# Optimization experiments

Hardware: AMD Instinct MI355X
Metric: run time of the kernel (lower is better)

## Reference

```python
import jax, jax.numpy as jnp
import numpy as np

DIM = 512
NUM_HEADS = 8
HEAD_DIM = DIM // NUM_HEADS
SCALE = HEAD_DIM ** -0.5
HIDDEN = int(DIM * 4.0)
LN_EPS = 1e-5


def layer_norm(x, w, b):
    mu = jnp.mean(x, axis=-1, keepdims=True)
    var = jnp.var(x, axis=-1, keepdims=True)
    return (x - mu) * jax.lax.rsqrt(var + LN_EPS) * w + b


def setup_inputs() -> dict:
    key = jax.random.key(0)
    ks = jax.random.split(key, 8)
    s = 0.02
    return {
        "x": jax.random.normal(ks[0], (8, 4096, DIM), dtype=jnp.float32),
        "ln1_w": jnp.ones((DIM,), jnp.float32),
        "ln1_b": jnp.zeros((DIM,), jnp.float32),
        "qkv_w": jax.random.normal(ks[1], (3 * DIM, DIM), jnp.float32) * s,
        "proj_w": jax.random.normal(ks[2], (DIM, DIM), jnp.float32) * s,
        "proj_b": jnp.zeros((DIM,), jnp.float32),
        "ln2_w": jnp.ones((DIM,), jnp.float32),
        "ln2_b": jnp.zeros((DIM,), jnp.float32),
        "fc1_w": jax.random.normal(ks[3], (HIDDEN, DIM), jnp.float32) * s,
        "fc1_b": jnp.zeros((HIDDEN,), jnp.float32),
        "fc2_w": jax.random.normal(ks[4], (DIM, HIDDEN), jnp.float32) * s,
        "fc2_b": jnp.zeros((DIM,), jnp.float32),
        "eca_w": jax.random.normal(ks[5], (1, 1, 3), jnp.float32) * 0.5,
    }


def channel_attention(x, qkv_w, proj_w, proj_b):
    B, N, C = x.shape
    qkv = (x @ qkv_w.T).reshape(B, N, 3, NUM_HEADS, HEAD_DIM)
    qkv = qkv.transpose(2, 0, 3, 1, 4)  # (3, B, h, N, hd)
    q, k, v = qkv[0], qkv[1] * SCALE, qkv[2]
    # cross-covariance attention: (hd x hd) per head
    attn = jax.nn.softmax(jnp.einsum("bhnd,bhne->bhde", k, v), axis=-1)
    out = jnp.einsum("bhde,bhne->bhnd", attn, q)  # (B, h, N, hd)
    out = out.transpose(0, 2, 1, 3).reshape(B, N, C)
    return out @ proj_w.T + proj_b


def mlp_eca(x, fc1_w, fc1_b, fc2_w, fc2_b, eca_w):
    B, N, C = x.shape
    H = W = int(np.sqrt(N))
    h = jax.nn.gelu(x @ fc1_w.T + fc1_b, approximate=False)
    y = h @ fc2_w.T + fc2_b  # (B, N, C)
    # faithful replication of torch .view(B, C, H, W) on contiguous (B, N, C)
    y4 = y.reshape(B, C, H, W)
    pooled = jnp.mean(y4, axis=(2, 3))  # (B, C)
    conv = jax.lax.conv_general_dilated(
        pooled[:, None, :], eca_w, window_strides=(1,), padding=[(1, 1)],
        dimension_numbers=("NCW", "OIW", "NCW"))[:, 0, :]  # (B, C)
    gate = jax.nn.sigmoid(conv)[:, :, None, None]
    y4 = y4 * gate + y4
    return y4.reshape(B, C, H * W).transpose(0, 2, 1)  # (B, N, C)


def reference(x, ln1_w, ln1_b, qkv_w, proj_w, proj_b, ln2_w, ln2_b,
              fc1_w, fc1_b, fc2_w, fc2_b, eca_w):
    cur = layer_norm(x, ln1_w, ln1_b)
    x = x + channel_attention(cur, qkv_w, proj_w, proj_b)
    x = x + mlp_eca(layer_norm(x, ln2_w, ln2_b), fc1_w, fc1_b, fc2_w, fc2_b, eca_w)
    return x
```

## Files before the change

kernel.cpp:

```cpp
#include <hip/hip_runtime.h>
#include <hip/hip_bf16.h>

typedef __bf16 bf16;
typedef __bf16 bf16x8 __attribute__((ext_vector_type(8)));
typedef float floatx4 __attribute__((ext_vector_type(4)));

#define B_    8
#define N_    4096
#define C_    512
#define BN_   32768
#define HID_  2048
#define SCALE_ 0.125f

__device__ __forceinline__ void load_lds16(const void* g, void* l) {
    __builtin_amdgcn_global_load_lds(
        (const __attribute__((address_space(1))) void*)g,
        (__attribute__((address_space(3))) void*)l, 16, 0, 0);
}

__device__ __forceinline__ float gelu_fast(float v) {
    float c = fmaf(v * v, 0.044715f, 1.0f) * v;
    float e = __builtin_amdgcn_exp2f(-2.3022082f * c);
    return v * __builtin_amdgcn_rcpf(1.0f + e);
}

__global__ void sniff_kernel(const unsigned int* __restrict__ xw, int* __restrict__ flag)
{
    int t = threadIdx.x;
    int votes = 0;
#pragma unroll
    for (int i = 0; i < 4; i++) {
        unsigned w = xw[t * 4 + i];
        if (w == 0u) continue;
        unsigned a = w & 0xFFFFu;
        unsigned e = (a >> 7) & 0xFFu;
        if (a != 0u && e >= 110u && e <= 135u) votes++; else votes--;
    }
#pragma unroll
    for (int off = 32; off; off >>= 1) votes += __shfl_xor(votes, off);
    __shared__ int s[4];
    if ((t & 63) == 0) s[t >> 6] = votes;
    __syncthreads();
    if (t == 0) *flag = (s[0] + s[1] + s[2] + s[3]) > 0 ? 1 : 0;
}

struct ConvArgs {
    const void* src[12];
    unsigned    dstoff[12];
    int         n[12];
};

__global__ __launch_bounds__(256) void convert_params(
    ConvArgs args, char* __restrict__ ws, const int* __restrict__ flag)
{
    int seg = blockIdx.y;
    int n = args.n[seg];
    int base = blockIdx.x * 2048;
    if (base >= n) return;
    bf16* dst = (bf16*)(ws + args.dstoff[seg]);
    const void* src = args.src[seg];
    bool isbf = (*flag != 0);
#pragma unroll
    for (int j = 0; j < 8; j++) {
        int idx = base + threadIdx.x + j * 256;
        if (idx < n) {
            float v = isbf ? (float)((const bf16*)src)[idx]
                           : ((const float*)src)[idx];
            dst[idx] = (bf16)v;
        }
    }
}

__device__ __forceinline__ void ln_core(float f[8], const bf16* w, const bf16* b,
                                        int lane, bf16* outp)
{
    float s = 0.f, sq = 0.f;
#pragma unroll
    for (int j = 0; j < 8; j++) { s += f[j]; sq += f[j]*f[j]; }
#pragma unroll
    for (int off = 32; off; off >>= 1) { s += __shfl_xor(s, off); sq += __shfl_xor(sq, off); }
    float mean = s * (1.f/512.f);
    float var  = sq * (1.f/512.f) - mean*mean;
    float inv  = rsqrtf(var + 1e-5f);
    bf16x8 wv = *(const bf16x8*)(w + lane*8);
    bf16x8 bv = *(const bf16x8*)(b + lane*8);
    bf16x8 o;
#pragma unroll
    for (int j = 0; j < 8; j++) o[j] = (bf16)((f[j]-mean)*inv*(float)wv[j] + (float)bv[j]);
    *(bf16x8*)outp = o;
}

__global__ __launch_bounds__(256) void ln_dyn_kernel(
    const void* __restrict__ xv, const bf16* __restrict__ w,
    const bf16* __restrict__ b, bf16* __restrict__ out, const int* __restrict__ flag)
{
    int wave = threadIdx.x >> 6, lane = threadIdx.x & 63;
    size_t row = (size_t)blockIdx.x * 4 + wave;
    float f[8];
    if (*flag) {
        bf16x8 v = *(const bf16x8*)((const bf16*)xv + row * C_ + lane * 8);
#pragma unroll
        for (int j = 0; j < 8; j++) f[j] = (float)v[j];
    } else {
        const float4* p = (const float4*)((const float*)xv + row * C_ + lane * 8);
        float4 v0 = p[0], v1 = p[1];
        f[0]=v0.x; f[1]=v0.y; f[2]=v0.z; f[3]=v0.w;
        f[4]=v1.x; f[5]=v1.y; f[6]=v1.z; f[7]=v1.w;
    }
    ln_core(f, w, b, lane, out + row * C_ + lane*8);
}

__global__ __launch_bounds__(256) void ln_b16_kernel(
    const bf16* __restrict__ x, const bf16* __restrict__ w,
    const bf16* __restrict__ b, bf16* __restrict__ out)
{
    int wave = threadIdx.x >> 6, lane = threadIdx.x & 63;
    size_t row = (size_t)blockIdx.x * 4 + wave;
    bf16x8 v = *(const bf16x8*)(x + row * C_ + lane * 8);
    float f[8];
#pragma unroll
    for (int j = 0; j < 8; j++) f[j] = (float)v[j];
    ln_core(f, w, b, lane, out + row * C_ + lane*8);
}

__global__ __launch_bounds__(256) void ln_f32_kernel(
    const float* __restrict__ x, const bf16* __restrict__ w,
    const bf16* __restrict__ b, bf16* __restrict__ out)
{
    int wave = threadIdx.x >> 6, lane = threadIdx.x & 63;
    size_t row = (size_t)blockIdx.x * 4 + wave;
    const float4* p = (const float4*)(x + row * C_ + lane * 8);
    float4 v0 = p[0], v1 = p[1];
    float f[8] = { v0.x, v0.y, v0.z, v0.w, v1.x, v1.y, v1.z, v1.w };
    ln_core(f, w, b, lane, out + row * C_ + lane*8);
}

enum { EPI_NONE = 0, EPI_BIAS = 1, EPI_BIAS_RESID = 2, EPI_BIAS_GELU = 3, EPI_QKV = 4 };

#define MM(AF, BF, AH, BH)                                                     \
    __builtin_amdgcn_s_setprio(1);                                             \
    _Pragma("unroll") for (int mi = 0; mi < 4; mi++)                           \
    _Pragma("unroll") for (int ni = 0; ni < 2; ni++)                           \
    _Pragma("unroll") for (int ks = 0; ks < 2; ks++)                           \
        acc[(AH)*4+mi][(BH)*2+ni] = __builtin_amdgcn_mfma_f32_16x16x32_bf16(   \
            AF[mi][ks], BF[ni][ks], acc[(AH)*4+mi][(BH)*2+ni], 0, 0, 0);       \
    __builtin_amdgcn_s_setprio(0);
#define STAGE2(GB, LB)                                                         \
    { load_lds16((GB) + goff0, (LB) + loff0);                                  \
      load_lds16((GB) + goff1, (LB) + loff1); }

#define KTILE(KT, S)                                                           \
{                                                                              \
    bf16x8 af[4][2], bf0[2][2], bf1[2][2];                                     \
                         \
    _Pragma("unroll") for (int mi = 0; mi < 4; mi++)                           \
    _Pragma("unroll") for (int ks = 0; ks < 2; ks++)                           \
        af[mi][ks] = *(const bf16x8*)(pa[mi][ks] + (S) * 16384);               \
    _Pragma("unroll") for (int ni = 0; ni < 2; ni++)                           \
    _Pragma("unroll") for (int ks = 0; ks < 2; ks++)                           \
        bf0[ni][ks] = *(const bf16x8*)(pb[ni][ks] + (S) * 16384);              \
    { const bf16* sp = ((KT) + 1 < NKT)                                        \
          ? A + (size_t)(m0 + 128) * K + (size_t)((KT) + 1) * 64               \
          : (hn ? A + (size_t)(m0n + 128) * K : nullptr);                      \
      if (sp) STAGE2(sp, &Asl[(S) ^ 1][1][0][0]); }                            \
    __builtin_amdgcn_s_barrier();                                              \
    asm volatile("s_waitcnt lgkmcnt(0)");                                      \
    __builtin_amdgcn_sched_barrier(0);                                         \
    MM(af, bf0, 0, 0)                                                          \
                             \
    _Pragma("unroll") for (int ni = 0; ni < 2; ni++)                           \
    _Pragma("unroll") for (int ks = 0; ks < 2; ks++)                           \
        bf1[ni][ks] = *(const bf16x8*)(pb[ni][ks] + (S) * 16384 + 8192);       \
    { const bf16* sp = ((KT) + 1 < NKT)                                        \
          ? W + (size_t)(n0 + 128) * K + (size_t)((KT) + 1) * 64               \
          : (hn ? W + (size_t)(n0n + 128) * K : nullptr);                      \
      if (sp) STAGE2(sp, &Bsl[(S) ^ 1][1][0][0]); }                            \
    __builtin_amdgcn_s_barrier();                                              \
    asm volatile("s_waitcnt lgkmcnt(0)");                                      \
    __builtin_amdgcn_sched_barrier(0);                                         \
    MM(af, bf1, 0, 1)                                                          \
                            \
    _Pragma("unroll") for (int mi = 0; mi < 4; mi++)                           \
    _Pragma("unroll") for (int ks = 0; ks < 2; ks++)                           \
        af[mi][ks] = *(const bf16x8*)(pa[mi][ks] + (S) * 16384 + 8192);        \
    { const bf16* sp = ((KT) + 2 < NKT)                                        \
          ? A + (size_t)m0 * K + (size_t)((KT) + 2) * 64                       \
          : (hn ? A + (size_t)m0n * K + (size_t)((KT) + 2 - NKT) * 64          \
               : nullptr);                                                     \
      if (sp) STAGE2(sp, &Asl[(S)][0][0][0]); }                                \
    __builtin_amdgcn_s_barrier();                                              \
    asm volatile("s_waitcnt lgkmcnt(0)");                                      \
    __builtin_amdgcn_sched_barrier(0);                                         \
    MM(af, bf1, 1, 1)                                                          \
               \
    { const bf16* sp = ((KT) + 2 < NKT)                                        \
          ? W + (size_t)n0 * K + (size_t)((KT) + 2) * 64                       \
          : (hn ? W + (size_t)n0n * K + (size_t)((KT) + 2 - NKT) * 64          \
               : nullptr);                                                     \
      if (sp) STAGE2(sp, &Bsl[(S)][0][0][0]); }                                \
    if ((KT) + 1 < NKT || hn) {                                                \
        if ((KT) + 2 < NKT || hn) asm volatile("s_waitcnt vmcnt(4)");          \
        else                      asm volatile("s_waitcnt vmcnt(0)");          \
    }                                                                          \
    __builtin_amdgcn_s_barrier();                                              \
    MM(af, bf0, 1, 0)                                                          \
}

template<typename OutT, int EPI>
__global__ __launch_bounds__(512, 2) void gemm256(
    const bf16* __restrict__ A, const bf16* __restrict__ W,
    const bf16* __restrict__ bias, const void* __restrict__ resid,
    const int* __restrict__ flag,
    OutT* __restrict__ Cout, bf16* __restrict__ Cout2, int M, int Nn, int K)
{
    __shared__ bf16 Asl[2][2][128][64];
    __shared__ bf16 Bsl[2][2][128][64];
    const int t = threadIdx.x;
    const int wv = t >> 6, lane = t & 63;
    const int quad = lane >> 4, l16 = lane & 15;
    const int wm = wv >> 2, wn = wv & 3;
    const int Nt = Nn >> 8;
    const int total = (M >> 8) * Nt;
    const int G = gridDim.x;
    const int NKT = K >> 6;

    const bf16* pa[4][2];
    const bf16* pb[2][2];
#pragma unroll
    for (int mi = 0; mi < 4; mi++) {
        int row = wm * 64 + mi * 16 + l16;
#pragma unroll
        for (int ks = 0; ks < 2; ks++)
            pa[mi][ks] = &Asl[0][0][0][0] + row * 64 +
                         ((ks * 32 + quad * 8) ^ ((row & 7) << 3));
    }
#pragma unroll
    for (int ni = 0; ni < 2; ni++) {
        int row = wn * 32 + ni * 16 + l16;
#pragma unroll
        for (int ks = 0; ks < 2; ks++)
            pb[ni][ks] = &Bsl[0][0][0][0] + row * 64 +
                         ((ks * 32 + quad * 8) ^ ((row & 7) << 3));
    }

    const int c0 = t, c1 = 512 + t;
    const int r0 = c0 >> 3, r1 = c1 >> 3;
    const size_t goff0 = (size_t)r0 * K + (size_t)(((c0 & 7) ^ (r0 & 7)) * 8);
    const size_t goff1 = (size_t)r1 * K + (size_t)(((c1 & 7) ^ (r1 & 7)) * 8);
    const int loff0 = c0 * 8, loff1 = c1 * 8;

    int id = blockIdx.x;
    if (id >= total) return;
    int m0 = (((id >> 3) / Nt) * 8 + (id & 7)) * 256;
    int n0 = ((id >> 3) % Nt) * 256;

    STAGE2(A + (size_t)m0 * K,         &Asl[0][0][0][0]);
    STAGE2(W + (size_t)n0 * K,         &Bsl[0][0][0][0]);
    STAGE2(A + (size_t)(m0 + 128) * K, &Asl[0][1][0][0]);
    STAGE2(W + (size_t)(n0 + 128) * K, &Bsl[0][1][0][0]);
    STAGE2(A + (size_t)m0 * K + 64,    &Asl[1][0][0][0]);
    STAGE2(W + (size_t)n0 * K + 64,    &Bsl[1][0][0][0]);
    asm volatile("s_waitcnt vmcnt(4)");
    __builtin_amdgcn_s_barrier();

    for (;;) {
        const int idn = id + G;
        const bool hn = idn < total;
        int m0n = 0, n0n = 0;
        if (hn) {
            m0n = (((idn >> 3) / Nt) * 8 + (idn & 7)) * 256;
            n0n = ((idn >> 3) % Nt) * 256;
        }

        floatx4 acc[8][4] = {};

        for (int kt = 0; kt < NKT; kt += 2) {
            KTILE(kt, 0)
            KTILE(kt + 1, 1)
        }

        size_t ldc = (size_t)Nn; int csub = 0; bool to2 = false;
        if (EPI == EPI_QKV) {
            if (n0 >= 512) { to2 = true; ldc = 1024; csub = 512; }
            else           { ldc = 512; }
        }
        bool isbf = false;
        if (EPI == EPI_BIAS_RESID) isbf = (*flag != 0);

#pragma unroll
        for (int mg = 0; mg < 8; mg++) {
            int rowg = m0 + (mg >> 2) * 128 + wm * 64 + (mg & 3) * 16 + quad * 4;
#pragma unroll
            for (int ng = 0; ng < 4; ng++) {
                int col = n0 + (ng >> 1) * 128 + wn * 32 + (ng & 1) * 16 + l16;
                float bv = (EPI == EPI_BIAS || EPI == EPI_BIAS_RESID || EPI == EPI_BIAS_GELU)
                           ? (float)bias[col] : 0.f;
#pragma unroll
                for (int r = 0; r < 4; r++) {
                    size_t idx = (size_t)(rowg + r) * ldc + (col - csub);
                    float v = acc[mg][ng][r] + bv;
                    if (EPI == EPI_BIAS_RESID) {
                        float rres = isbf ? (float)((const bf16*)resid)[idx]
                                          : ((const float*)resid)[idx];
                        v += rres;
                    }
                    if (EPI == EPI_BIAS_GELU)  v = gelu_fast(v);
                    if (EPI == EPI_QKV && to2) Cout2[idx] = (bf16)v;
                    else                       Cout[idx]  = (OutT)v;
                }
            }
        }

        if (!hn) break;
        id = idn; m0 = m0n; n0 = n0n;
    }
}

__global__ __launch_bounds__(256) void attn_logits_mfma(
    const bf16* __restrict__ kv, float* __restrict__ partial)
{
    __shared__ bf16 Kt[64][136];
    __shared__ bf16 Vt[64][136];
    int s = blockIdx.x, bh = blockIdx.y, b = bh >> 3, h = bh & 7;
    int t = threadIdx.x, wave = t >> 6, lane = t & 63;
    int quad = lane >> 4, l16 = lane & 15;
    floatx4 acc[4] = {};
    for (int c = 0; c < 4; c++) {
        int n0 = s * 512 + c * 128;
        {
            int isv = t >> 7;
            int r   = t & 127;
            const bf16* gp = &kv[((size_t)b * N_ + n0 + r) * 1024 + h * 64 + isv * 512];
            bf16x8 rowv[8];
#pragma unroll
            for (int u = 0; u < 8; u++) rowv[u] = *(const bf16x8*)(gp + u * 8);
            bf16 (*dst)[136] = isv ? Vt : Kt;
#pragma unroll
            for (int u = 0; u < 8; u++)
#pragma unroll
                for (int jj = 0; jj < 8; jj++)
                    dst[u * 8 + jj][r] = rowv[u][jj];
        }
        __syncthreads();
#pragma unroll
        for (int ks = 0; ks < 4; ks++) {
            bf16x8 af = *(const bf16x8*)&Kt[wave * 16 + l16][ks * 32 + quad * 8];
#pragma unroll
            for (int ni = 0; ni < 4; ni++) {
                bf16x8 bfv = *(const bf16x8*)&Vt[ni * 16 + l16][ks * 32 + quad * 8];
                acc[ni] = __builtin_amdgcn_mfma_f32_16x16x32_bf16(af, bfv, acc[ni], 0, 0, 0);
            }
        }
        __syncthreads();
    }
    float* p = partial + ((size_t)bh * 8 + s) * 4096;
#pragma unroll
    for (int ni = 0; ni < 4; ni++)
#pragma unroll
        for (int r = 0; r < 4; r++)
            p[(wave * 16 + quad * 4 + r) * 64 + ni * 16 + l16] = acc[ni][r];
}

__global__ __launch_bounds__(256) void attn_softmax_kernel(
    const float* __restrict__ partial, bf16* __restrict__ attnb)
{
    int bh = blockIdx.y;
    int wave = threadIdx.x >> 6, lane = threadIdx.x & 63;
    for (int r = 0; r < 4; r++) {
        int d = blockIdx.x * 16 + wave * 4 + r;
        float v = 0.f;
#pragma unroll
        for (int s = 0; s < 8; s++) v += partial[((size_t)bh*8 + s)*4096 + d*64 + lane];
        v *= SCALE_;
        float m = v;
#pragma unroll
        for (int off = 32; off; off >>= 1) m = fmaxf(m, __shfl_xor(m, off));
        float p = expf(v - m);
        float sum = p;
#pragma unroll
        for (int off = 32; off; off >>= 1) sum += __shfl_xor(sum, off);
        attnb[(size_t)bh*4096 + d*64 + lane] = (bf16)(p / sum);
    }
}

__global__ __launch_bounds__(256) void attn_apply_mfma(
    const bf16* __restrict__ q, const bf16* __restrict__ attnb,
    bf16* __restrict__ outT)
{
    int bh = blockIdx.y, b = bh >> 3, h = bh & 7;
    int t = threadIdx.x, wave = t >> 6, lane = t & 63;
    int quad = lane >> 4, l16 = lane & 15;
    int nbase = blockIdx.x * 256 + wave * 64;
    bf16x8 bfrag[4][2];
#pragma unroll
    for (int di = 0; di < 4; di++)
#pragma unroll
        for (int ks = 0; ks < 2; ks++)
            bfrag[di][ks] = *(const bf16x8*)&attnb[(size_t)bh*4096 + (di*16 + l16)*64 + ks*32 + quad*8];
    floatx4 acc[4][4] = {};
#pragma unroll
    for (int mi = 0; mi < 4; mi++) {
#pragma unroll
        for (int ks = 0; ks < 2; ks++) {
            bf16x8 af = *(const bf16x8*)&q[((size_t)b*N_ + nbase + mi*16 + l16)*512 + h*64 + ks*32 + quad*8];
#pragma unroll
            for (int di = 0; di < 4; di++)
                acc[mi][di] = __builtin_amdgcn_mfma_f32_16x16x32_bf16(af, bfrag[di][ks], acc[mi][di], 0, 0, 0);
        }
    }
#pragma unroll
    for (int mi = 0; mi < 4; mi++)
#pragma unroll
        for (int di = 0; di < 4; di++)
#pragma unroll
            for (int r = 0; r < 4; r++)
                outT[((size_t)b*N_ + nbase + mi*16 + quad*4 + r)*512 + h*64 + di*16 + l16] =
                    (bf16)acc[mi][di][r];
}

__global__ __launch_bounds__(256) void pooled_kernel(
    const bf16* __restrict__ y, float* __restrict__ pooled)
{
    int bc = blockIdx.x;
    const bf16* p = y + (size_t)bc * 4096 + threadIdx.x * 16;
    float s = 0.f;
#pragma unroll
    for (int i = 0; i < 2; i++) {
        bf16x8 v = *(const bf16x8*)(p + i*8);
#pragma unroll
        for (int j = 0; j < 8; j++) s += (float)v[j];
    }
#pragma unroll
    for (int off = 32; off; off >>= 1) s += __shfl_xor(s, off);
    __shared__ float red[4];
    if ((threadIdx.x & 63) == 0) red[threadIdx.x >> 6] = s;
    __syncthreads();
    if (threadIdx.x == 0)
        pooled[bc] = (red[0] + red[1] + red[2] + red[3]) * (1.f/4096.f);
}

__global__ void gate_kernel(const float* __restrict__ pooled,
                            const bf16* __restrict__ eca_w, float* __restrict__ gate1)
{
    int c = threadIdx.x, b = blockIdx.x;
    float w0 = (float)eca_w[0], w1 = (float)eca_w[1], w2 = (float)eca_w[2];
    const float* p = pooled + b * 512;
    float conv = w1 * p[c];
    if (c > 0)   conv += w0 * p[c-1];
    if (c < 511) conv += w2 * p[c+1];
    float g = 1.f / (1.f + expf(-conv));
    gate1[b * 512 + c] = 1.f + g;
}

__global__ __launch_bounds__(256) void final_rmw(
    const bf16* __restrict__ y, const float* __restrict__ gate1,
    float* __restrict__ out)
{
    int b = blockIdx.z, c0 = blockIdx.y * 64, n0 = blockIdx.x * 64;
    __shared__ float ytile[64][65];
    int t = threadIdx.x;
#pragma unroll
    for (int i = 0; i < 2; i++) {
        int chunk = t * 2 + i;
        int ci = chunk >> 3, nj = (chunk & 7) * 8;
        bf16x8 v = *(const bf16x8*)&y[(size_t)b * ((size_t)N_*C_) + (size_t)(c0+ci) * 4096 + n0 + nj];
#pragma unroll
        for (int j = 0; j < 8; j++) ytile[ci][nj+j] = (float)v[j];
    }
    __syncthreads();
    int cc = t & 63, nb = t >> 6;
    float g = gate1[b * 512 + c0 + cc];
    for (int p = 0; p < 16; p++) {
        int nr = p * 4 + nb;
        size_t idx = ((size_t)b * N_ + n0 + nr) * C_ + c0 + cc;
        out[idx] = out[idx] + g * ytile[cc][nr];
    }
}

__global__ __launch_bounds__(256) void final_fresh(
    const bf16* __restrict__ y, const bf16* __restrict__ x2b,
    const float* __restrict__ gate1, float* __restrict__ out)
{
    int b = blockIdx.z, c0 = blockIdx.y * 64, n0 = blockIdx.x * 64;
    __shared__ float ytile[64][65];
    int t = threadIdx.x;
#pragma unroll
    for (int i = 0; i < 2; i++) {
        int chunk = t * 2 + i;
        int ci = chunk >> 3, nj = (chunk & 7) * 8;
        bf16x8 v = *(const bf16x8*)&y[(size_t)b * ((size_t)N_*C_) + (size_t)(c0+ci) * 4096 + n0 + nj];
#pragma unroll
        for (int j = 0; j < 8; j++) ytile[ci][nj+j] = (float)v[j];
    }
    __syncthreads();
    int cc = t & 63, nb = t >> 6;
    float g = gate1[b * 512 + c0 + cc];
    for (int p = 0; p < 16; p++) {
        int nr = p * 4 + nb;
        size_t idx = ((size_t)b * N_ + n0 + nr) * C_ + c0 + cc;
        out[idx] = (float)x2b[idx] + g * ytile[cc][nr];
    }
}

extern "C" void kernel_launch(void* const* d_in, const int* in_sizes, int n_in,
                              void* d_out, int out_size, void* d_ws, size_t ws_size,
                              hipStream_t stream)
{
    float* outf = (float*)d_out;
    bf16*  outb = (bf16*)d_out;
    char* ws = (char*)d_ws;

    int*   flag    = (int*)ws;
    float* pooled  = (float*)(ws + 4096);
    float* gate1   = (float*)(ws + 20480);
    bf16* ln1_w = (bf16*)(ws + 65536);
    bf16* ln1_b = (bf16*)(ws + 67584);
    bf16* ln2_w = (bf16*)(ws + 69632);
    bf16* ln2_b = (bf16*)(ws + 71680);
    bf16* proj_b= (bf16*)(ws + 73728);
    bf16* fc2_b = (bf16*)(ws + 75776);
    bf16* eca_w = (bf16*)(ws + 77824);
    bf16* fc1_b = (bf16*)(ws + 81920);
    bf16* qkv_w = (bf16*)(ws + ((size_t)1 << 20));
    bf16* proj_w= (bf16*)(ws + (size_t)2621440);
    bf16* fc1_w = (bf16*)(ws + ((size_t)3 << 20));
    bf16* fc2_w = (bf16*)(ws + ((size_t)5 << 20));
    float* partial = (float*)(ws + ((size_t)7  << 20));
    bf16*  attnb   = (bf16*)(ws + ((size_t)15 << 20));
    bf16*  T1      = (bf16*)(ws + ((size_t)16 << 20));
    bf16*  kvbuf   = (bf16*)(ws + ((size_t)48 << 20));
    bf16*  hbuf    = kvbuf;
    bf16*  x2b     = (bf16*)(ws + ((size_t)176 << 20));

    const bool fat = ws_size >= ((size_t)212 << 20);

    sniff_kernel<<<1, 256, 0, stream>>>((const unsigned int*)d_in[0], flag);

    ConvArgs ca;
    const int   srcidx[12] = { 1, 2, 6, 7, 5, 11, 12, 9, 3, 4, 8, 10 };
    const unsigned offs[12] = { 65536, 67584, 69632, 71680, 73728, 75776, 77824, 81920,
                                1u<<20, 2621440u, 3u<<20, 5u<<20 };
    for (int i = 0; i < 12; i++) {
        ca.src[i] = d_in[srcidx[i]];
        ca.dstoff[i] = offs[i];
        ca.n[i] = in_sizes[srcidx[i]];
    }
    convert_params<<<dim3(512, 12), 256, 0, stream>>>(ca, ws, flag);

    ln_dyn_kernel<<<BN_/4, 256, 0, stream>>>(d_in[0], ln1_w, ln1_b, T1, flag);

    gemm256<bf16, EPI_QKV><<<256, 512, 0, stream>>>(
        T1, qkv_w, nullptr, nullptr, flag, outb, kvbuf, BN_, 1536, 512);

    attn_logits_mfma<<<dim3(8, 64), 256, 0, stream>>>(kvbuf, partial);
    attn_softmax_kernel<<<dim3(4, 64), 256, 0, stream>>>(partial, attnb);
    attn_apply_mfma<<<dim3(16, 64), 256, 0, stream>>>(outb, attnb, T1);

    if (fat) {
        gemm256<bf16, EPI_BIAS_RESID><<<256, 512, 0, stream>>>(
            T1, proj_w, proj_b, d_in[0], flag, x2b, nullptr, BN_, 512, 512);
        ln_b16_kernel<<<BN_/4, 256, 0, stream>>>(x2b, ln2_w, ln2_b, T1);
        gemm256<bf16, EPI_BIAS_GELU><<<256, 512, 0, stream>>>(
            T1, fc1_w, fc1_b, nullptr, flag, hbuf, nullptr, BN_, 2048, 512);
        gemm256<bf16, EPI_BIAS><<<256, 512, 0, stream>>>(
            hbuf, fc2_w, fc2_b, nullptr, flag, T1, nullptr, BN_, 512, 2048);
        pooled_kernel<<<4096, 256, 0, stream>>>(T1, pooled);
        gate_kernel<<<8, 512, 0, stream>>>(pooled, eca_w, gate1);
        final_fresh<<<dim3(64, 8, 8), 256, 0, stream>>>(T1, x2b, gate1, outf);
    } else {
        gemm256<float, EPI_BIAS_RESID><<<256, 512, 0, stream>>>(
            T1, proj_w, proj_b, d_in[0], flag, outf, nullptr, BN_, 512, 512);
        ln_f32_kernel<<<BN_/4, 256, 0, stream>>>(outf, ln2_w, ln2_b, T1);
        for (int ch = 0; ch < 2; ch++) {
            bf16* Tch = T1 + (size_t)ch * 16384 * 512;
            gemm256<bf16, EPI_BIAS_GELU><<<256, 512, 0, stream>>>(
                Tch, fc1_w, fc1_b, nullptr, flag, hbuf, nullptr, 16384, 2048, 512);
            gemm256<bf16, EPI_BIAS><<<128, 512, 0, stream>>>(
                hbuf, fc2_w, fc2_b, nullptr, flag, Tch, nullptr, 16384, 512, 2048);
        }
        pooled_kernel<<<4096, 256, 0, stream>>>(T1, pooled);
        gate_kernel<<<8, 512, 0, stream>>>(pooled, eca_w, gate1);
        final_rmw<<<dim3(64, 8, 8), 256, 0, stream>>>(T1, gate1, outf);
    }
}
```

Before: 521.9 us.

## Software-pipeline LDS fragment loads across MFMA phases and stage bf16 epilogue through LDS

The GEMM k-tile loop now double-buffers A fragments (even/odd) and preloads the next tile's A and B fragments during the current MFMA phases. This removes the explicit lgkmcnt(0) waits before each MFMA group so LDS reads overlap with matrix math. The non-residual epilogues also go through a small per-wave LDS staging buffer, which turns scattered 2-byte bf16 stores into 16-byte vector stores. In exchange it uses more registers and extra LDS, and it depends on the compiler inserting correct waits for the fragment loads.

Result: no change. 513.1 us (-1.7%).

```diff
diff --git a/kernel.cpp b/kernel.cpp
--- a/kernel.cpp
+++ b/kernel.cpp
@@ -151,48 +151,37 @@
 
 #define KTILE(KT, S)                                                           \
 {                                                                              \
-    bf16x8 af[4][2], bf0[2][2], bf1[2][2];                                     \
-                         \
-    _Pragma("unroll") for (int mi = 0; mi < 4; mi++)                           \
-    _Pragma("unroll") for (int ks = 0; ks < 2; ks++)                           \
-        af[mi][ks] = *(const bf16x8*)(pa[mi][ks] + (S) * 16384);               \
-    _Pragma("unroll") for (int ni = 0; ni < 2; ni++)                           \
-    _Pragma("unroll") for (int ks = 0; ks < 2; ks++)                           \
-        bf0[ni][ks] = *(const bf16x8*)(pb[ni][ks] + (S) * 16384);              \
+                      \
     { const bf16* sp = ((KT) + 1 < NKT)                                        \
           ? A + (size_t)(m0 + 128) * K + (size_t)((KT) + 1) * 64               \
           : (hn ? A + (size_t)(m0n + 128) * K : nullptr);                      \
       if (sp) STAGE2(sp, &Asl[(S) ^ 1][1][0][0]); }                            \
     __builtin_amdgcn_s_barrier();                                              \
-    asm volatile("s_waitcnt lgkmcnt(0)");                                      \
-    __builtin_amdgcn_sched_barrier(0);                                         \
-    MM(af, bf0, 0, 0)                                                          \
-                             \
     _Pragma("unroll") for (int ni = 0; ni < 2; ni++)                           \
     _Pragma("unroll") for (int ks = 0; ks < 2; ks++)                           \
         bf1[ni][ks] = *(const bf16x8*)(pb[ni][ks] + (S) * 16384 + 8192);       \
+    __builtin_amdgcn_sched_barrier(0);                                         \
+    MM(afE, bf0, 0, 0)                                                         \
+                      \
     { const bf16* sp = ((KT) + 1 < NKT)                                        \
           ? W + (size_t)(n0 + 128) * K + (size_t)((KT) + 1) * 64               \
           : (hn ? W + (size_t)(n0n + 128) * K : nullptr);                      \
       if (sp) STAGE2(sp, &Bsl[(S) ^ 1][1][0][0]); }                            \
     __builtin_amdgcn_s_barrier();                                              \
-    asm volatile("s_waitcnt lgkmcnt(0)");                                      \
-    __builtin_amdgcn_sched_barrier(0);                                         \
-    MM(af, bf1, 0, 1)                                                          \
-                            \
     _Pragma("unroll") for (int mi = 0; mi < 4; mi++)                           \
     _Pragma("unroll") for (int ks = 0; ks < 2; ks++)                           \
-        af[mi][ks] = *(const bf16x8*)(pa[mi][ks] + (S) * 16384 + 8192);        \
+        afO[mi][ks] = *(const bf16x8*)(pa[mi][ks] + (S) * 16384 + 8192);       \
+    __builtin_amdgcn_sched_barrier(0);                                         \
+    MM(afE, bf1, 0, 1)                                                         \
+                                      \
     { const bf16* sp = ((KT) + 2 < NKT)                                        \
           ? A + (size_t)m0 * K + (size_t)((KT) + 2) * 64                       \
           : (hn ? A + (size_t)m0n * K + (size_t)((KT) + 2 - NKT) * 64          \
                : nullptr);                                                     \
       if (sp) STAGE2(sp, &Asl[(S)][0][0][0]); }                                \
     __builtin_amdgcn_s_barrier();                                              \
-    asm volatile("s_waitcnt lgkmcnt(0)");                                      \
-    __builtin_amdgcn_sched_barrier(0);                                         \
-    MM(af, bf1, 1, 1)                                                          \
-               \
+    MM(afO, bf1, 1, 1)                                                         \
+                                                        \
     { const bf16* sp = ((KT) + 2 < NKT)                                        \
           ? W + (size_t)n0 * K + (size_t)((KT) + 2) * 64                       \
           : (hn ? W + (size_t)n0n * K + (size_t)((KT) + 2 - NKT) * 64          \
@@ -203,7 +192,19 @@
         else                      asm volatile("s_waitcnt vmcnt(0)");          \
     }                                                                          \
     __builtin_amdgcn_s_barrier();                                              \
-    MM(af, bf0, 1, 0)                                                          \
+    if ((KT) + 1 < NKT || hn) {                                                \
+        _Pragma("unroll") for (int mi = 0; mi < 4; mi++)                       \
+        _Pragma("unroll") for (int ks = 0; ks < 2; ks++)                       \
+            afE[mi][ks] = *(const bf16x8*)(pa[mi][ks] + ((S) ^ 1) * 16384);    \
+    }                                                                          \
+    __builtin_amdgcn_sched_barrier(0);                                         \
+    MM(afO, bf0, 1, 0)                                                         \
+    if ((KT) + 1 < NKT || hn) {                                                \
+        _Pragma("unroll") for (int ni = 0; ni < 2; ni++)                       \
+        _Pragma("unroll") for (int ks = 0; ks < 2; ks++)                       \
+            bf0[ni][ks] = *(const bf16x8*)(pb[ni][ks] + ((S) ^ 1) * 16384);    \
+    }                                                                          \
+    __builtin_amdgcn_sched_barrier(0);                                         \
 }
 
 template<typename OutT, int EPI>
@@ -215,6 +216,7 @@
 {
     __shared__ bf16 Asl[2][2][128][64];
     __shared__ bf16 Bsl[2][2][128][64];
+    __shared__ bf16 EpiL[8][16][66];
     const int t = threadIdx.x;
     const int wv = t >> 6, lane = t & 63;
     const int quad = lane >> 4, l16 = lane & 15;
@@ -263,6 +265,18 @@
     asm volatile("s_waitcnt vmcnt(4)");
     __builtin_amdgcn_s_barrier();
 
+    bf16x8 afE[4][2], afO[4][2], bf0[2][2], bf1[2][2];
+#pragma unroll
+    for (int mi = 0; mi < 4; mi++)
+#pragma unroll
+        for (int ks = 0; ks < 2; ks++)
+            afE[mi][ks] = *(const bf16x8*)(pa[mi][ks]);
+#pragma unroll
+    for (int ni = 0; ni < 2; ni++)
+#pragma unroll
+        for (int ks = 0; ks < 2; ks++)
+            bf0[ni][ks] = *(const bf16x8*)(pb[ni][ks]);
+
     for (;;) {
         const int idn = id + G;
         const bool hn = idn < total;
@@ -279,34 +293,56 @@
             KTILE(kt + 1, 1)
         }
 
-        size_t ldc = (size_t)Nn; int csub = 0; bool to2 = false;
-        if (EPI == EPI_QKV) {
-            if (n0 >= 512) { to2 = true; ldc = 1024; csub = 512; }
-            else           { ldc = 512; }
-        }
-        bool isbf = false;
-        if (EPI == EPI_BIAS_RESID) isbf = (*flag != 0);
-
-#pragma unroll
-        for (int mg = 0; mg < 8; mg++) {
-            int rowg = m0 + (mg >> 2) * 128 + wm * 64 + (mg & 3) * 16 + quad * 4;
-#pragma unroll
-            for (int ng = 0; ng < 4; ng++) {
-                int col = n0 + (ng >> 1) * 128 + wn * 32 + (ng & 1) * 16 + l16;
-                float bv = (EPI == EPI_BIAS || EPI == EPI_BIAS_RESID || EPI == EPI_BIAS_GELU)
-                           ? (float)bias[col] : 0.f;
-#pragma unroll
-                for (int r = 0; r < 4; r++) {
-                    size_t idx = (size_t)(rowg + r) * ldc + (col - csub);
-                    float v = acc[mg][ng][r] + bv;
-                    if (EPI == EPI_BIAS_RESID) {
+        if constexpr (EPI != EPI_BIAS_RESID) {
+            bf16* epi = &EpiL[wv][0][0];
+            const int rl = lane >> 2, cg = lane & 3;
+#pragma unroll
+            for (int mg = 0; mg < 8; mg++) {
+#pragma unroll
+                for (int ng = 0; ng < 4; ng++) {
+                    int col = n0 + (ng >> 1) * 128 + wn * 32 + (ng & 1) * 16 + l16;
+                    float bv = (EPI == EPI_BIAS || EPI == EPI_BIAS_GELU)
+                               ? (float)bias[col] : 0.f;
+                    int cc2 = (ng >> 1) * 32 + (ng & 1) * 16 + l16;
+#pragma unroll
+                    for (int r = 0; r < 4; r++) {
+                        float v = acc[mg][ng][r] + bv;
+                        if (EPI == EPI_BIAS_GELU) v = gelu_fast(v);
+                        epi[(quad * 4 + r) * 66 + cc2] = (bf16)v;
+                    }
+                }
+                bf16x8 v0 = *(const bf16x8*)(epi + rl * 66 + cg * 16);
+                bf16x8 v1 = *(const bf16x8*)(epi + rl * 66 + cg * 16 + 8);
+                int rowg = m0 + (mg >> 2) * 128 + wm * 64 + (mg & 3) * 16 + rl;
+                int colg = n0 + (cg >> 1) * 128 + wn * 32 + (cg & 1) * 16;
+                bf16* dst;
+                if (EPI == EPI_QKV && colg >= 512)
+                    dst = Cout2 + (size_t)rowg * 1024 + (colg - 512);
+                else if (EPI == EPI_QKV)
+                    dst = (bf16*)(void*)Cout + (size_t)rowg * 512 + colg;
+                else
+                    dst = (bf16*)(void*)Cout + (size_t)rowg * (size_t)Nn + colg;
+                *(bf16x8*)dst = v0;
+                *(bf16x8*)(dst + 8) = v1;
+            }
+        } else {
+            bool isbf = (*flag != 0);
+#pragma unroll
+            for (int mg = 0; mg < 8; mg++) {
+                int rowg = m0 + (mg >> 2) * 128 + wm * 64 + (mg & 3) * 16 + quad * 4;
+#pragma unroll
+                for (int ng = 0; ng < 4; ng++) {
+                    int col = n0 + (ng >> 1) * 128 + wn * 32 + (ng & 1) * 16 + l16;
+                    float bv = (float)bias[col];
+#pragma unroll
+                    for (int r = 0; r < 4; r++) {
+                        size_t idx = (size_t)(rowg + r) * (size_t)Nn + col;
+                        float v = acc[mg][ng][r] + bv;
                         float rres = isbf ? (float)((const bf16*)resid)[idx]
                                           : ((const float*)resid)[idx];
                         v += rres;
+                        Cout[idx] = (OutT)v;
                     }
-                    if (EPI == EPI_BIAS_GELU)  v = gelu_fast(v);
-                    if (EPI == EPI_QKV && to2) Cout2[idx] = (bf16)v;
-                    else                       Cout[idx]  = (OutT)v;
                 }
             }
         }
```
